# Performance work log

Hardware: AMD Instinct MI355X
Metric: run time of the kernel (lower is better)

The kernel has to match this reference:

```python
import jax, jax.numpy as jnp
import numpy as np
from jax.scipy.special import logsumexp

VOCAB, EMB, SEQ = 100000, 300, 32768
NTAGS = 14          # 12 real tags + START + STOP
START, STOP = 12, 13
NEG = -10000.0


def setup_inputs() -> dict:
    key = jax.random.key(0)
    k0, k1, k2, k3, k4 = jax.random.split(key, 5)
    sentence = jax.random.randint(k0, (SEQ,), 0, VOCAB, dtype=jnp.int32)
    tags = jax.random.randint(k1, (SEQ,), 0, 12, dtype=jnp.int32)  # real tags only
    embeddings = jax.random.normal(k2, (VOCAB, EMB), dtype=jnp.float32)
    W = jax.random.normal(k3, (NTAGS, EMB), dtype=jnp.float32)  # linear2tag, no bias
    transitions = jax.random.normal(k4, (NTAGS, NTAGS), dtype=jnp.float32)
    # match __init__: no transition into START, none out of STOP
    transitions = transitions.at[START, :].set(NEG).at[:, STOP].set(NEG)
    return {"sentence": sentence, "tags": tags, "embeddings": embeddings,
            "W": W, "transitions": transitions}


def _forward_alg(feats, transitions):
    # feats: [L, T]; transitions[next, prev]
    init = jnp.full((NTAGS,), NEG, feats.dtype).at[START].set(0.0)

    def step(fv, feat):
        # alphas[next, prev] = fv[prev] + trans[next, prev] + feat[next]
        alphas = fv[None, :] + transitions + feat[:, None]
        return logsumexp(alphas, axis=1), None

    fv, _ = jax.lax.scan(step, init, feats)
    return logsumexp(fv + transitions[STOP])


def _score_sentence(feats, transitions, tags):
    prev = jnp.concatenate([jnp.array([START], tags.dtype), tags[:-1]])
    trans_score = jnp.sum(transitions[tags, prev])
    emit_score = jnp.sum(jnp.take_along_axis(feats, tags[:, None].astype(jnp.int32), axis=1))
    return trans_score + emit_score + transitions[STOP, tags[-1]]


def _viterbi(feats, transitions):
    init = jnp.full((NTAGS,), NEG, feats.dtype).at[START].set(0.0)

    def step(fv, feat):
        nv = fv[None, :] + transitions          # [next, prev]
        bp = jnp.argmax(nv, axis=1)             # best prev for each next
        return jnp.max(nv, axis=1) + feat, bp

    fv, bps = jax.lax.scan(step, init, feats)   # bps: [L, T]
    terminal = fv + transitions[STOP]
    best_last = jnp.argmax(terminal)
    path_score = terminal[best_last]

    def back(tag, bp):
        return bp[tag], tag                     # emit tag at this position

    _, path = jax.lax.scan(back, best_last, bps, reverse=True)  # [L]
    return path_score, path


def reference(sentence, tags, embeddings, W, transitions):
    # _get_features: embedding lookup + bias-free linear to tag space
    feats = embeddings[sentence] @ W.T                     # [L, T]
    forward_score = _forward_alg(feats, transitions)
    gold_score = _score_sentence(feats, transitions, tags)
    nll = forward_score - gold_score                       # neg_log_likelihood
    path_score, best_path = _viterbi(feats, transitions)   # module.forward
    return nll, path_score, best_path
```

## Files before the change

kernel.cpp:

```cpp
#include <hip/hip_runtime.h>


#define LSEQ    32768
#define NTAGS   14
#define R       12
#define T_START 12
#define T_STOP  13
#define EMBD    300
#define CCH     2048
#define SCH     16
#define NSUP    128
#define NHYP    8

#define OFF_FEATS 0
#define OFF_EXPF  393216
#define OFF_FMAX  786432
#define OFF_PF    819200
#define OFF_PV    1114112
#define OFF_PVC   1409024
#define OFF_BV    1703936
#define OFF_SFX   1728512
#define OFF_GOLD  1753088
#define OFF_SMV   1753104
#define OFF_SMVT  1771536
#define OFF_SMF   1789968
#define OFF_HMV   1808400
#define OFF_HMVT  1809552
#define OFF_HMF   1810704
#define OFF_SBV   1811856
#define OFF_SSFX  1813392
#define OFF_HBV   1814928
#define OFF_HSFX  1815024

__device__ __forceinline__ void load12(const float* __restrict__ p, float* r) {
  const float4* p4 = (const float4*)p;
  float4 a = p4[0], b = p4[1], c = p4[2];
  r[0]=a.x; r[1]=a.y; r[2]=a.z; r[3]=a.w;
  r[4]=b.x; r[5]=b.y; r[6]=b.z; r[7]=b.w;
  r[8]=c.x; r[9]=c.y; r[10]=c.z; r[11]=c.w;
}

__device__ __forceinline__ void lds12(const float* p, float* r) {
  const float4* p4 = (const float4*)p;
  float4 a = p4[0], b = p4[1], c = p4[2];
  r[0]=a.x; r[1]=a.y; r[2]=a.z; r[3]=a.w;
  r[4]=b.x; r[5]=b.y; r[6]=b.z; r[7]=b.w;
  r[8]=c.x; r[9]=c.y; r[10]=c.z; r[11]=c.w;
}

__global__ __launch_bounds__(256) void k_feats(
    const int* __restrict__ sentence, const int* __restrict__ tags,
    const float* __restrict__ emb, const float* __restrict__ W,
    const float* __restrict__ trans, float* __restrict__ ws)
{
  __shared__ float Wl[NTAGS * EMBD];
  __shared__ float gacc;
  for (int i = threadIdx.x; i < NTAGS * EMBD; i += 256) Wl[i] = W[i];
  if (threadIdx.x == 0) gacc = 0.f;
  __syncthreads();

  int grp = threadIdx.x >> 4;
  int g   = threadIdx.x & 15;
  int pos = blockIdx.x * 16 + grp;
  int row = sentence[pos];

  float acc = 0.f;
  if (g < R) {
    const float4* e4 = (const float4*)(emb + (size_t)row * EMBD);
    const float4* w4 = (const float4*)(Wl + g * EMBD);
    #pragma unroll 5
    for (int i = 0; i < EMBD / 4; ++i) {
      float4 a = e4[i]; float4 b = w4[i];
      acc += a.x*b.x + a.y*b.y + a.z*b.z + a.w*b.w;
    }
  }
  float feat = (g < R) ? acc : -3.0e38f;
  float mx = feat;
  #pragma unroll
  for (int off = 1; off < 16; off <<= 1)
    mx = fmaxf(mx, __shfl_xor(mx, off, 16));

  if (g < R) {
    ws[OFF_FEATS + pos * 12 + g] = feat;
    ws[OFF_EXPF  + pos * 12 + g] = __expf(feat - mx);
  }
  if (g == 0) ws[OFF_FMAX + pos] = mx;

  int tg = tags[pos];
  if (g == tg) {
    int prev = (pos == 0) ? T_START : tags[pos - 1];
    float gc = feat + trans[tg * NTAGS + prev];
    if (pos == LSEQ - 1) gc += trans[T_STOP * NTAGS + tg];
    atomicAdd(&gacc, gc);
  }
  __syncthreads();
  if (threadIdx.x == 0) atomicAdd(&ws[OFF_GOLD], gacc);
}

__global__ __launch_bounds__(64) void k_pass1(
    const float* __restrict__ trans, float* __restrict__ ws)
{
  int role = blockIdx.x >> 9;
  int q = threadIdx.x >> 4;
  int p = threadIdx.x & 15;
  int c = (blockIdx.x & 511) * 4 + q;
  int t0 = (c == 0) ? 1 : c * SCH;
  int t1 = c * SCH + SCH;
  bool act = (p < R);

  float Treg[R][R];

  if (role == 0) {
    #pragma unroll
    for (int n = 0; n < R; ++n)
      #pragma unroll
      for (int m = 0; m < R; ++m)
        Treg[n][m] = __expf(trans[n * NTAGS + m]);

    float E[R];
    #pragma unroll
    for (int m = 0; m < R; ++m) E[m] = (m == p) ? 1.f : 0.f;
    int kacc = 0;
    float sfeat = 0.f;

    float ef[R];
    load12(ws + OFF_EXPF + t0 * 12, ef);
    float fm = ws[OFF_FMAX + t0];

    for (int t = t0; t < t1; ++t) {
      float efn[R];
      load12(ws + OFF_EXPF + (t + 1) * 12, efn);
      float fmn = ws[OFF_FMAX + t + 1];
      sfeat += fm;
      float NE[R];
      #pragma unroll
      for (int n = 0; n < R; ++n) {
        float s = Treg[n][0] * E[0];
        #pragma unroll
        for (int m = 1; m < R; ++m) s = fmaf(Treg[n][m], E[m], s);
        NE[n] = s * ef[n];
      }
      #pragma unroll
      for (int n = 0; n < R; ++n) E[n] = NE[n];
      if ((t & 7) == 7) {
        float mx = E[0];
        #pragma unroll
        for (int n = 1; n < R; ++n) mx = fmaxf(mx, E[n]);
        if (mx > 0.f) {
          int k = ((__float_as_int(mx) >> 23) & 0xFF) - 127;
          float sc = __int_as_float((127 - k) << 23);
          #pragma unroll
          for (int n = 0; n < R; ++n) E[n] *= sc;
          kacc += k;
        }
      }
      #pragma unroll
      for (int n = 0; n < R; ++n) ef[n] = efn[n];
      fm = fmn;
    }
    if (act) {
      float base = (float)kacc * 0.6931471805599453f + sfeat;
      #pragma unroll
      for (int n = 0; n < R; ++n) {
        float v = (E[n] > 0.f) ? (__logf(E[n]) + base) : -1.0e30f;
        ws[OFF_PF + c * 144 + n * 12 + p] = v;
      }
    }
  } else {
    #pragma unroll
    for (int n = 0; n < R; ++n)
      #pragma unroll
      for (int m = 0; m < R; ++m)
        Treg[n][m] = trans[n * NTAGS + m];

    float V[R];
    #pragma unroll
    for (int m = 0; m < R; ++m) V[m] = (m == p) ? 0.f : -1.0e30f;

    float fr[R];
    load12(ws + OFF_FEATS + t0 * 12, fr);

    for (int t = t0; t < t1; ++t) {
      float frn[R];
      load12(ws + OFF_FEATS + (t + 1) * 12, frn);
      float NV[R];
      #pragma unroll
      for (int n = 0; n < R; ++n) {
        float b = Treg[n][0] + V[0];
        #pragma unroll
        for (int m = 1; m < R; ++m) b = fmaxf(b, Treg[n][m] + V[m]);
        NV[n] = b + fr[n];
      }
      #pragma unroll
      for (int n = 0; n < R; ++n) { V[n] = NV[n]; fr[n] = frn[n]; }
    }
    if (act) {
      #pragma unroll
      for (int n = 0; n < R; ++n) {
        ws[OFF_PV  + c * 144 + n * 12 + p] = V[n];
        ws[OFF_PVC + c * 144 + p * 12 + n] = V[n];
      }
    }
  }
}

__global__ __launch_bounds__(192) void k_fold(
    float* __restrict__ ws, int srcV, int srcF, int dstV, int dstVT, int dstF)
{
  __shared__ float Ml[144];
  __shared__ float Vl[144];
  int s   = blockIdx.x >> 1;
  int sem = blockIdx.x & 1;
  int l = threadIdx.x;
  bool act = (l < 144);
  int n = l / 12;
  int p = l - n * 12;
  int base = sem ? srcF : srcV;

  float V = (act && n == p) ? 0.f : -1.0e30f;
  float mreg = act ? ws[base + (s * 16) * 144 + l] : 0.f;

  for (int j = 0; j < 16; ++j) {
    if (act) { Ml[l] = mreg; Vl[l] = V; }
    __syncthreads();
    if (act) mreg = ws[base + (s * 16 + j + 1) * 144 + l];
    if (act) {
      if (sem == 0) {
        float best = -3.0e38f;
        #pragma unroll
        for (int m = 0; m < R; ++m)
          best = fmaxf(best, Ml[n * 12 + m] + Vl[m * 12 + p]);
        V = best;
      } else {
        float cand[R]; float mx = -3.0e38f;
        #pragma unroll
        for (int m = 0; m < R; ++m) {
          cand[m] = Ml[n * 12 + m] + Vl[m * 12 + p];
          mx = fmaxf(mx, cand[m]);
        }
        float sum = 0.f;
        #pragma unroll
        for (int m = 0; m < R; ++m) sum += __expf(cand[m] - mx);
        V = mx + __logf(sum);
      }
    }
    __syncthreads();
  }
  if (act) {
    if (sem == 0) {
      ws[dstV  + s * 144 + n * 12 + p] = V;
      ws[dstVT + s * 144 + p * 12 + n] = V;
    } else {
      ws[dstF + s * 144 + n * 12 + p] = V;
    }
  }
}

__global__ __launch_bounds__(192) void k_mid(
    const float* __restrict__ trans, float* __restrict__ ws,
    float* __restrict__ out)
{
  __shared__ float Vsh[3][16];
  int wid  = threadIdx.x >> 6;
  int lane = threadIdx.x & 63;
  int n = lane;
  bool act = (n < R);

  if (wid == 0) {
    float x = -3.0e38f;
    if (act) {
      x = trans[n * NTAGS + T_START] + ws[OFF_FEATS + n];
      ws[OFF_HBV + n] = x;
      Vsh[0][n] = x;
    }
    float row[R], rown[R];
    if (act) load12(ws + OFF_HMV + n * 12, row);
    for (int h = 0; h < NHYP; ++h) {
      if (act) load12(ws + OFF_HMV + (h + 1) * 144 + n * 12, rown);
      float v[R];
      lds12(Vsh[0], v);
      if (act) {
        float nx = row[0] + v[0];
        #pragma unroll
        for (int m = 1; m < R; ++m) nx = fmaxf(nx, row[m] + v[m]);
        if (h < NHYP - 1) ws[OFF_HBV + (h + 1) * 12 + n] = nx;
        Vsh[0][n] = nx;
        #pragma unroll
        for (int m = 0; m < R; ++m) row[m] = rown[m];
      }
    }
    if (lane == 0) {
      float v[R];
      lds12(Vsh[0], v);
      float ps = -3.0e38f;
      #pragma unroll
      for (int m = 0; m < R; ++m) ps = fmaxf(ps, v[m] + trans[T_STOP * NTAGS + m]);
      out[1] = ps;
    }
  } else if (wid == 1) {
    float x = -3.0e38f;
    if (act) {
      x = trans[T_STOP * NTAGS + n];
      ws[OFF_HSFX + (NHYP - 1) * 12 + n] = x;
      Vsh[1][n] = x;
    }
    float row[R], rown[R];
    if (act) load12(ws + OFF_HMVT + (NHYP - 1) * 144 + n * 12, row);
    for (int h = NHYP - 1; h >= 1; --h) {
      if (act) load12(ws + OFF_HMVT + (h - 1) * 144 + n * 12, rown);
      float v[R];
      lds12(Vsh[1], v);
      if (act) {
        float nx = row[0] + v[0];
        #pragma unroll
        for (int m = 1; m < R; ++m) nx = fmaxf(nx, row[m] + v[m]);
        ws[OFF_HSFX + (h - 1) * 12 + n] = nx;
        Vsh[1][n] = nx;
        #pragma unroll
        for (int m = 0; m < R; ++m) row[m] = rown[m];
      }
    }
  } else if (wid == 2) {
    float x = -3.0e38f;
    if (act) {
      x = trans[n * NTAGS + T_START] + ws[OFF_FEATS + n];
      Vsh[2][n] = x;
    }
    float row[R], rown[R];
    if (act) load12(ws + OFF_HMF + n * 12, row);
    for (int h = 0; h < NHYP; ++h) {
      if (act) load12(ws + OFF_HMF + (h + 1) * 144 + n * 12, rown);
      float v[R];
      lds12(Vsh[2], v);
      if (act) {
        float tv[R]; float mx = -3.0e38f;
        #pragma unroll
        for (int m = 0; m < R; ++m) { tv[m] = row[m] + v[m]; mx = fmaxf(mx, tv[m]); }
        float sum = 0.f;
        #pragma unroll
        for (int m = 0; m < R; ++m) sum += __expf(tv[m] - mx);
        Vsh[2][n] = mx + __logf(sum);
        #pragma unroll
        for (int m = 0; m < R; ++m) row[m] = rown[m];
      }
    }
    if (lane == 0) {
      float v[R];
      lds12(Vsh[2], v);
      float mx = -3.0e38f;
      #pragma unroll
      for (int m = 0; m < R; ++m) mx = fmaxf(mx, v[m] + trans[T_STOP * NTAGS + m]);
      float sum = 0.f;
      #pragma unroll
      for (int m = 0; m < R; ++m) sum += __expf(v[m] + trans[T_STOP * NTAGS + m] - mx);
      out[0] = (mx + __logf(sum)) - ws[OFF_GOLD];
    }
  }
}

__global__ __launch_bounds__(64) void k_expandA(
    float* __restrict__ ws)
{
  __shared__ float Vsh[4][16];
  int q = threadIdx.x >> 4;
  int g = threadIdx.x & 15;
  int task = blockIdx.x * 4 + q;
  int h = task >> 1;
  int dir = task & 1;
  bool act = (g < R);

  if (dir == 0) {
    float x = -3.0e38f;
    if (act) {
      x = ws[OFF_HBV + h * 12 + g];
      ws[OFF_SBV + (h * 16) * 12 + g] = x;
      Vsh[q][g] = x;
    }
    float row[R], rown[R];
    if (act) load12(ws + OFF_SMV + (h * 16) * 144 + g * 12, row);
    for (int j = 0; j < 15; ++j) {
      int s = h * 16 + j;
      if (act) load12(ws + OFF_SMV + (s + 1) * 144 + g * 12, rown);
      float v[R];
      lds12(Vsh[q], v);
      if (act) {
        float nx = row[0] + v[0];
        #pragma unroll
        for (int m = 1; m < R; ++m) nx = fmaxf(nx, row[m] + v[m]);
        ws[OFF_SBV + (s + 1) * 12 + g] = nx;
        Vsh[q][g] = nx;
        #pragma unroll
        for (int m = 0; m < R; ++m) row[m] = rown[m];
      }
    }
  } else {
    float x = -3.0e38f;
    if (act) {
      x = ws[OFF_HSFX + h * 12 + g];
      ws[OFF_SSFX + (h * 16 + 15) * 12 + g] = x;
      Vsh[q][g] = x;
    }
    float row[R], rown[R];
    if (act) load12(ws + OFF_SMVT + (h * 16 + 15) * 144 + g * 12, row);
    for (int j = 15; j >= 1; --j) {
      int s = h * 16 + j;
      if (act) load12(ws + OFF_SMVT + (s - 1) * 144 + g * 12, rown);
      float v[R];
      lds12(Vsh[q], v);
      if (act) {
        float nx = row[0] + v[0];
        #pragma unroll
        for (int m = 1; m < R; ++m) nx = fmaxf(nx, row[m] + v[m]);
        ws[OFF_SSFX + (s - 1) * 12 + g] = nx;
        Vsh[q][g] = nx;
        #pragma unroll
        for (int m = 0; m < R; ++m) row[m] = rown[m];
      }
    }
  }
}

__global__ __launch_bounds__(64) void k_expandB(
    float* __restrict__ ws)
{
  __shared__ float Vsh[4][16];
  int q = threadIdx.x >> 4;
  int g = threadIdx.x & 15;
  int task = blockIdx.x * 4 + q;
  int s = task >> 1;
  int dir = task & 1;
  bool act = (g < R);

  if (dir == 0) {
    float x = -3.0e38f;
    if (act) {
      x = ws[OFF_SBV + s * 12 + g];
      ws[OFF_BV + (s * 16) * 12 + g] = x;
      Vsh[q][g] = x;
    }
    float row[R], rown[R];
    if (act) load12(ws + OFF_PV + (s * 16) * 144 + g * 12, row);
    for (int j = 0; j < 15; ++j) {
      int c = s * 16 + j;
      if (act) load12(ws + OFF_PV + (c + 1) * 144 + g * 12, rown);
      float v[R];
      lds12(Vsh[q], v);
      if (act) {
        float nx = row[0] + v[0];
        #pragma unroll
        for (int m = 1; m < R; ++m) nx = fmaxf(nx, row[m] + v[m]);
        ws[OFF_BV + (c + 1) * 12 + g] = nx;
        Vsh[q][g] = nx;
        #pragma unroll
        for (int m = 0; m < R; ++m) row[m] = rown[m];
      }
    }
  } else {
    float x = -3.0e38f;
    if (act) {
      x = ws[OFF_SSFX + s * 12 + g];
      ws[OFF_SFX + (s * 16 + 15) * 12 + g] = x;
      Vsh[q][g] = x;
    }
    float row[R], rown[R];
    if (act) load12(ws + OFF_PVC + (s * 16 + 15) * 144 + g * 12, row);
    for (int j = 15; j >= 1; --j) {
      int c = s * 16 + j;
      if (act) load12(ws + OFF_PVC + (c - 1) * 144 + g * 12, rown);
      float v[R];
      lds12(Vsh[q], v);
      if (act) {
        float nx = row[0] + v[0];
        #pragma unroll
        for (int m = 1; m < R; ++m) nx = fmaxf(nx, row[m] + v[m]);
        ws[OFF_SFX + (c - 1) * 12 + g] = nx;
        Vsh[q][g] = nx;
        #pragma unroll
        for (int m = 0; m < R; ++m) row[m] = rown[m];
      }
    }
  }
}

__global__ __launch_bounds__(64) void k_decode(
    const float* __restrict__ trans, const float* __restrict__ ws,
    float* __restrict__ out)
{
  __shared__ unsigned char bp[4][SCH][16];
  __shared__ float Vsh[4][16];
  int q = threadIdx.x >> 4;
  int g = threadIdx.x & 15;
  int c = blockIdx.x * 4 + q;
  int t0 = (c == 0) ? 1 : c * SCH;
  int t1 = c * SCH + SCH;
  bool act = (g < R);

  float treg[R];
  #pragma unroll
  for (int m = 0; m < R; ++m) treg[m] = act ? trans[g * NTAGS + m] : 0.f;

  float fv = act ? ws[OFF_BV + c * 12 + g] : -3.0e38f;
  Vsh[q][g] = fv;
  float fc = ws[OFF_FEATS + t0 * 12 + g];

  for (int t = t0; t < t1; ++t) {
    float fn = ws[OFF_FEATS + (t + 1) * 12 + g];
    float v[R];
    lds12(Vsh[q], v);
    float best = -3.0e38f; int bi = 0;
    #pragma unroll
    for (int m = 0; m < R; ++m) {
      float cand = treg[m] + v[m];
      if (cand > best) { best = cand; bi = m; }
    }
    float nfv = best + fc;
    if (act) {
      bp[q][t - t0][g] = (unsigned char)bi;
      Vsh[q][g] = nfv;
    }
    fc = fn;
  }

  Vsh[q][g] = act ? (Vsh[q][g] + ws[OFF_SFX + c * 12 + g]) : -3.0e38f;

  if (g == 0) {
    float best = Vsh[q][0]; int idx = 0;
    #pragma unroll
    for (int m = 1; m < R; ++m) {
      float v = Vsh[q][m];
      if (v > best) { best = v; idx = m; }
    }
    int cur = idx;
    int len = t1 - t0;
    out[2 + t0 + len - 1] = (float)cur;
    for (int tt = len - 1; tt >= 1; --tt) {
      cur = bp[q][tt][cur];
      out[2 + t0 + tt - 1] = (float)cur;
    }
    if (c == 0) {
      cur = bp[q][0][cur];
      out[2 + 0] = (float)cur;
    }
  }
}

extern "C" void kernel_launch(void* const* d_in, const int* in_sizes, int n_in,
                              void* d_out, int out_size, void* d_ws, size_t ws_size,
                              hipStream_t stream) {
  (void)in_sizes; (void)n_in; (void)out_size; (void)ws_size;
  const int*   sentence = (const int*)d_in[0];
  const int*   tags     = (const int*)d_in[1];
  const float* emb      = (const float*)d_in[2];
  const float* W        = (const float*)d_in[3];
  const float* trans    = (const float*)d_in[4];
  float* ws  = (float*)d_ws;
  float* out = (float*)d_out;

  hipMemsetAsync(ws + OFF_GOLD, 0, sizeof(float), stream);
  k_feats<<<LSEQ / 16, 256, 0, stream>>>(sentence, tags, emb, W, trans, ws);
  k_pass1<<<1024, 64, 0, stream>>>(trans, ws);
  k_fold<<<NSUP * 2, 192, 0, stream>>>(ws, OFF_PV, OFF_PF, OFF_SMV, OFF_SMVT, OFF_SMF);
  k_fold<<<NHYP * 2, 192, 0, stream>>>(ws, OFF_SMV, OFF_SMF, OFF_HMV, OFF_HMVT, OFF_HMF);
  k_mid<<<1, 192, 0, stream>>>(trans, ws, out);
  k_expandA<<<4, 64, 0, stream>>>(ws);
  k_expandB<<<64, 64, 0, stream>>>(ws);
  k_decode<<<CCH / 4, 64, 0, stream>>>(trans, ws, out);
}
```

Baseline: 274.0 us.

## Fuse post-feature CRF stages into one cooperative kernel with grid syncs

Replaces the seven kernel launches after feature computation (pass1, two folds, mid, two expands, decode) with a single cooperative kernel of 256 blocks that separates the stages with grid.sync(). The gold-score atomic plus its memset are replaced by per-block partial sums that one block reduces inside the mega kernel. The aim is to remove launch gaps and tail latency between many tiny serial kernels. In exchange, grid-wide barriers add their own cost, and the fold stages now run with fewer, larger blocks. The old multi-kernel path is kept as a fallback if the cooperative launch fails.

```diff
diff --git a/kernel.cpp b/kernel.cpp
--- a/kernel.cpp
+++ b/kernel.cpp
@@ -1,4 +1,7 @@
 #include <hip/hip_runtime.h>
+#include <hip/hip_cooperative_groups.h>
+
+namespace cg = cooperative_groups;
 
 
 #define LSEQ    32768
@@ -31,6 +34,7 @@
 #define OFF_SSFX  1813392
 #define OFF_HBV   1814928
 #define OFF_HSFX  1815024
+#define OFF_GOLDP 1815120
 
 __device__ __forceinline__ void load12(const float* __restrict__ p, float* r) {
   const float4* p4 = (const float4*)p;
@@ -94,7 +98,495 @@
     atomicAdd(&gacc, gc);
   }
   __syncthreads();
-  if (threadIdx.x == 0) atomicAdd(&ws[OFF_GOLD], gacc);
+  if (threadIdx.x == 0) ws[OFF_GOLDP + blockIdx.x] = gacc;
+}
+
+__device__ __forceinline__ void fold16(
+    float* __restrict__ ws, float* Ml, float* Vl, int tid, int s, int sem,
+    int srcV, int srcF, int dstV, int dstVT, int dstF)
+{
+  int l = tid;
+  bool act = (l < 144);
+  int n = l / 12;
+  int p = l - n * 12;
+  int base = sem ? srcF : srcV;
+
+  float V = (act && n == p) ? 0.f : -1.0e30f;
+  float mreg = act ? ws[base + (s * 16) * 144 + l] : 0.f;
+
+  for (int j = 0; j < 16; ++j) {
+    if (act) { Ml[l] = mreg; Vl[l] = V; }
+    __syncthreads();
+    if (act) mreg = ws[base + (s * 16 + j + 1) * 144 + l];
+    if (act) {
+      if (sem == 0) {
+        float best = -3.0e38f;
+        #pragma unroll
+        for (int m = 0; m < R; ++m)
+          best = fmaxf(best, Ml[n * 12 + m] + Vl[m * 12 + p]);
+        V = best;
+      } else {
+        float cand[R]; float mx = -3.0e38f;
+        #pragma unroll
+        for (int m = 0; m < R; ++m) {
+          cand[m] = Ml[n * 12 + m] + Vl[m * 12 + p];
+          mx = fmaxf(mx, cand[m]);
+        }
+        float sum = 0.f;
+        #pragma unroll
+        for (int m = 0; m < R; ++m) sum += __expf(cand[m] - mx);
+        V = mx + __logf(sum);
+      }
+    }
+    __syncthreads();
+  }
+  if (act) {
+    if (sem == 0) {
+      ws[dstV  + s * 144 + n * 12 + p] = V;
+      ws[dstVT + s * 144 + p * 12 + n] = V;
+    } else {
+      ws[dstF + s * 144 + n * 12 + p] = V;
+    }
+  }
+}
+
+__global__ __launch_bounds__(256) void k_mega(
+    const float* __restrict__ trans, float* __restrict__ ws,
+    float* __restrict__ out)
+{
+  cg::grid_group grid = cg::this_grid();
+  const int tid = threadIdx.x;
+  const int bid = blockIdx.x;
+
+  __shared__ float Ml[144];
+  __shared__ float Vl[144];
+  __shared__ float Vmid[3][16];
+  __shared__ float VexA[4][16];
+  __shared__ float VexB[4][16];
+  __shared__ float Vdec[8][16];
+  __shared__ unsigned char bpd[8][SCH][16];
+  __shared__ float gsh[256];
+
+  {
+    int gw   = bid * 4 + (tid >> 6);
+    int lane = tid & 63;
+    int role = gw >> 9;
+    int q = lane >> 4;
+    int p = lane & 15;
+    int c = (gw & 511) * 4 + q;
+    int t0 = (c == 0) ? 1 : c * SCH;
+    int t1 = c * SCH + SCH;
+    bool act = (p < R);
+
+    float Treg[R][R];
+
+    if (role == 0) {
+      #pragma unroll
+      for (int n = 0; n < R; ++n)
+        #pragma unroll
+        for (int m = 0; m < R; ++m)
+          Treg[n][m] = __expf(trans[n * NTAGS + m]);
+
+      float E[R];
+      #pragma unroll
+      for (int m = 0; m < R; ++m) E[m] = (m == p) ? 1.f : 0.f;
+      int kacc = 0;
+      float sfeat = 0.f;
+
+      float ef[R];
+      load12(ws + OFF_EXPF + t0 * 12, ef);
+      float fm = ws[OFF_FMAX + t0];
+
+      for (int t = t0; t < t1; ++t) {
+        float efn[R];
+        load12(ws + OFF_EXPF + (t + 1) * 12, efn);
+        float fmn = ws[OFF_FMAX + t + 1];
+        sfeat += fm;
+        float NE[R];
+        #pragma unroll
+        for (int n = 0; n < R; ++n) {
+          float s = Treg[n][0] * E[0];
+          #pragma unroll
+          for (int m = 1; m < R; ++m) s = fmaf(Treg[n][m], E[m], s);
+          NE[n] = s * ef[n];
+        }
+        #pragma unroll
+        for (int n = 0; n < R; ++n) E[n] = NE[n];
+        if ((t & 7) == 7) {
+          float mx = E[0];
+          #pragma unroll
+          for (int n = 1; n < R; ++n) mx = fmaxf(mx, E[n]);
+          if (mx > 0.f) {
+            int k = ((__float_as_int(mx) >> 23) & 0xFF) - 127;
+            float sc = __int_as_float((127 - k) << 23);
+            #pragma unroll
+            for (int n = 0; n < R; ++n) E[n] *= sc;
+            kacc += k;
+          }
+        }
+        #pragma unroll
+        for (int n = 0; n < R; ++n) ef[n] = efn[n];
+        fm = fmn;
+      }
+      if (act) {
+        float base = (float)kacc * 0.6931471805599453f + sfeat;
+        #pragma unroll
+        for (int n = 0; n < R; ++n) {
+          float v = (E[n] > 0.f) ? (__logf(E[n]) + base) : -1.0e30f;
+          ws[OFF_PF + c * 144 + n * 12 + p] = v;
+        }
+      }
+    } else {
+      #pragma unroll
+      for (int n = 0; n < R; ++n)
+        #pragma unroll
+        for (int m = 0; m < R; ++m)
+          Treg[n][m] = trans[n * NTAGS + m];
+
+      float V[R];
+      #pragma unroll
+      for (int m = 0; m < R; ++m) V[m] = (m == p) ? 0.f : -1.0e30f;
+
+      float fr[R];
+      load12(ws + OFF_FEATS + t0 * 12, fr);
+
+      for (int t = t0; t < t1; ++t) {
+        float frn[R];
+        load12(ws + OFF_FEATS + (t + 1) * 12, frn);
+        float NV[R];
+        #pragma unroll
+        for (int n = 0; n < R; ++n) {
+          float b = Treg[n][0] + V[0];
+          #pragma unroll
+          for (int m = 1; m < R; ++m) b = fmaxf(b, Treg[n][m] + V[m]);
+          NV[n] = b + fr[n];
+        }
+        #pragma unroll
+        for (int n = 0; n < R; ++n) { V[n] = NV[n]; fr[n] = frn[n]; }
+      }
+      if (act) {
+        #pragma unroll
+        for (int n = 0; n < R; ++n) {
+          ws[OFF_PV  + c * 144 + n * 12 + p] = V[n];
+          ws[OFF_PVC + c * 144 + p * 12 + n] = V[n];
+        }
+      }
+    }
+  }
+  grid.sync();
+
+  fold16(ws, Ml, Vl, tid, bid >> 1, bid & 1,
+         OFF_PV, OFF_PF, OFF_SMV, OFF_SMVT, OFF_SMF);
+  grid.sync();
+
+  if (bid < 16) {
+    fold16(ws, Ml, Vl, tid, bid >> 1, bid & 1,
+           OFF_SMV, OFF_SMF, OFF_HMV, OFF_HMVT, OFF_HMF);
+  } else if (bid == 16) {
+    float s = 0.f;
+    for (int i = tid; i < CCH; i += 256) s += ws[OFF_GOLDP + i];
+    gsh[tid] = s;
+    __syncthreads();
+    for (int off = 128; off > 0; off >>= 1) {
+      if (tid < off) gsh[tid] += gsh[tid + off];
+      __syncthreads();
+    }
+    if (tid == 0) ws[OFF_GOLD] = gsh[0];
+  }
+  grid.sync();
+
+  if (bid == 0) {
+    int wid  = tid >> 6;
+    int lane = tid & 63;
+    int n = lane;
+    bool act = (n < R);
+
+    if (wid == 0) {
+      float x = -3.0e38f;
+      if (act) {
+        x = trans[n * NTAGS + T_START] + ws[OFF_FEATS + n];
+        ws[OFF_HBV + n] = x;
+        Vmid[0][n] = x;
+      }
+      float row[R], rown[R];
+      if (act) load12(ws + OFF_HMV + n * 12, row);
+      for (int h = 0; h < NHYP; ++h) {
+        if (act) load12(ws + OFF_HMV + (h + 1) * 144 + n * 12, rown);
+        float v[R];
+        lds12(Vmid[0], v);
+        if (act) {
+          float nx = row[0] + v[0];
+          #pragma unroll
+          for (int m = 1; m < R; ++m) nx = fmaxf(nx, row[m] + v[m]);
+          if (h < NHYP - 1) ws[OFF_HBV + (h + 1) * 12 + n] = nx;
+          Vmid[0][n] = nx;
+          #pragma unroll
+          for (int m = 0; m < R; ++m) row[m] = rown[m];
+        }
+      }
+      if (lane == 0) {
+        float v[R];
+        lds12(Vmid[0], v);
+        float ps = -3.0e38f;
+        #pragma unroll
+        for (int m = 0; m < R; ++m) ps = fmaxf(ps, v[m] + trans[T_STOP * NTAGS + m]);
+        out[1] = ps;
+      }
+    } else if (wid == 1) {
+      float x = -3.0e38f;
+      if (act) {
+        x = trans[T_STOP * NTAGS + n];
+        ws[OFF_HSFX + (NHYP - 1) * 12 + n] = x;
+        Vmid[1][n] = x;
+      }
+      float row[R], rown[R];
+      if (act) load12(ws + OFF_HMVT + (NHYP - 1) * 144 + n * 12, row);
+      for (int h = NHYP - 1; h >= 1; --h) {
+        if (act) load12(ws + OFF_HMVT + (h - 1) * 144 + n * 12, rown);
+        float v[R];
+        lds12(Vmid[1], v);
+        if (act) {
+          float nx = row[0] + v[0];
+          #pragma unroll
+          for (int m = 1; m < R; ++m) nx = fmaxf(nx, row[m] + v[m]);
+          ws[OFF_HSFX + (h - 1) * 12 + n] = nx;
+          Vmid[1][n] = nx;
+          #pragma unroll
+          for (int m = 0; m < R; ++m) row[m] = rown[m];
+        }
+      }
+    } else if (wid == 2) {
+      float x = -3.0e38f;
+      if (act) {
+        x = trans[n * NTAGS + T_START] + ws[OFF_FEATS + n];
+        Vmid[2][n] = x;
+      }
+      float row[R], rown[R];
+      if (act) load12(ws + OFF_HMF + n * 12, row);
+      for (int h = 0; h < NHYP; ++h) {
+        if (act) load12(ws + OFF_HMF + (h + 1) * 144 + n * 12, rown);
+        float v[R];
+        lds12(Vmid[2], v);
+        if (act) {
+          float tv[R]; float mx = -3.0e38f;
+          #pragma unroll
+          for (int m = 0; m < R; ++m) { tv[m] = row[m] + v[m]; mx = fmaxf(mx, tv[m]); }
+          float sum = 0.f;
+          #pragma unroll
+          for (int m = 0; m < R; ++m) sum += __expf(tv[m] - mx);
+          Vmid[2][n] = mx + __logf(sum);
+          #pragma unroll
+          for (int m = 0; m < R; ++m) row[m] = rown[m];
+        }
+      }
+      if (lane == 0) {
+        float v[R];
+        lds12(Vmid[2], v);
+        float mx = -3.0e38f;
+        #pragma unroll
+        for (int m = 0; m < R; ++m) mx = fmaxf(mx, v[m] + trans[T_STOP * NTAGS + m]);
+        float sum = 0.f;
+        #pragma unroll
+        for (int m = 0; m < R; ++m) sum += __expf(v[m] + trans[T_STOP * NTAGS + m] - mx);
+        out[0] = (mx + __logf(sum)) - ws[OFF_GOLD];
+      }
+    }
+  }
+  grid.sync();
+
+  if (bid < 4 && tid < 64) {
+    int q = tid >> 4;
+    int g = tid & 15;
+    int task = bid * 4 + q;
+    int h = task >> 1;
+    int dir = task & 1;
+    bool act = (g < R);
+
+    if (dir == 0) {
+      float x = -3.0e38f;
+      if (act) {
+        x = ws[OFF_HBV + h * 12 + g];
+        ws[OFF_SBV + (h * 16) * 12 + g] = x;
+        VexA[q][g] = x;
+      }
+      float row[R], rown[R];
+      if (act) load12(ws + OFF_SMV + (h * 16) * 144 + g * 12, row);
+      for (int j = 0; j < 15; ++j) {
+        int s = h * 16 + j;
+        if (act) load12(ws + OFF_SMV + (s + 1) * 144 + g * 12, rown);
+        float v[R];
+        lds12(VexA[q], v);
+        if (act) {
+          float nx = row[0] + v[0];
+          #pragma unroll
+          for (int m = 1; m < R; ++m) nx = fmaxf(nx, row[m] + v[m]);
+          ws[OFF_SBV + (s + 1) * 12 + g] = nx;
+          VexA[q][g] = nx;
+          #pragma unroll
+          for (int m = 0; m < R; ++m) row[m] = rown[m];
+        }
+      }
+    } else {
+      float x = -3.0e38f;
+      if (act) {
+        x = ws[OFF_HSFX + h * 12 + g];
+        ws[OFF_SSFX + (h * 16 + 15) * 12 + g] = x;
+        VexA[q][g] = x;
+      }
+      float row[R], rown[R];
+      if (act) load12(ws + OFF_SMVT + (h * 16 + 15) * 144 + g * 12, row);
+      for (int j = 15; j >= 1; --j) {
+        int s = h * 16 + j;
+        if (act) load12(ws + OFF_SMVT + (s - 1) * 144 + g * 12, rown);
+        float v[R];
+        lds12(VexA[q], v);
+        if (act) {
+          float nx = row[0] + v[0];
+          #pragma unroll
+          for (int m = 1; m < R; ++m) nx = fmaxf(nx, row[m] + v[m]);
+          ws[OFF_SSFX + (s - 1) * 12 + g] = nx;
+          VexA[q][g] = nx;
+          #pragma unroll
+          for (int m = 0; m < R; ++m) row[m] = rown[m];
+        }
+      }
+    }
+  }
+  grid.sync();
+
+  if (bid < 64 && tid < 64) {
+    int q = tid >> 4;
+    int g = tid & 15;
+    int task = bid * 4 + q;
+    int s = task >> 1;
+    int dir = task & 1;
+    bool act = (g < R);
+
+    if (dir == 0) {
+      float x = -3.0e38f;
+      if (act) {
+        x = ws[OFF_SBV + s * 12 + g];
+        ws[OFF_BV + (s * 16) * 12 + g] = x;
+        VexB[q][g] = x;
+      }
+      float row[R], rown[R];
+      if (act) load12(ws + OFF_PV + (s * 16) * 144 + g * 12, row);
+      for (int j = 0; j < 15; ++j) {
+        int c = s * 16 + j;
+        if (act) load12(ws + OFF_PV + (c + 1) * 144 + g * 12, rown);
+        float v[R];
+        lds12(VexB[q], v);
+        if (act) {
+          float nx = row[0] + v[0];
+          #pragma unroll
+          for (int m = 1; m < R; ++m) nx = fmaxf(nx, row[m] + v[m]);
+          ws[OFF_BV + (c + 1) * 12 + g] = nx;
+          VexB[q][g] = nx;
+          #pragma unroll
+          for (int m = 0; m < R; ++m) row[m] = rown[m];
+        }
+      }
+    } else {
+      float x = -3.0e38f;
+      if (act) {
+        x = ws[OFF_SSFX + s * 12 + g];
+        ws[OFF_SFX + (s * 16 + 15) * 12 + g] = x;
+        VexB[q][g] = x;
+      }
+      float row[R], rown[R];
+      if (act) load12(ws + OFF_PVC + (s * 16 + 15) * 144 + g * 12, row);
+      for (int j = 15; j >= 1; --j) {
+        int c = s * 16 + j;
+        if (act) load12(ws + OFF_PVC + (c - 1) * 144 + g * 12, rown);
+        float v[R];
+        lds12(VexB[q], v);
+        if (act) {
+          float nx = row[0] + v[0];
+          #pragma unroll
+          for (int m = 1; m < R; ++m) nx = fmaxf(nx, row[m] + v[m]);
+          ws[OFF_SFX + (c - 1) * 12 + g] = nx;
+          VexB[q][g] = nx;
+          #pragma unroll
+          for (int m = 0; m < R; ++m) row[m] = rown[m];
+        }
+      }
+    }
+  }
+  grid.sync();
+
+  {
+    int q = tid >> 4;
+    int g = tid & 15;
+    if (q < 8) {
+      int c = bid * 8 + q;
+      int t0 = (c == 0) ? 1 : c * SCH;
+      int t1 = c * SCH + SCH;
+      bool act = (g < R);
+
+      float treg[R];
+      #pragma unroll
+      for (int m = 0; m < R; ++m) treg[m] = act ? trans[g * NTAGS + m] : 0.f;
+
+      float fv = act ? ws[OFF_BV + c * 12 + g] : -3.0e38f;
+      Vdec[q][g] = fv;
+      float fc = ws[OFF_FEATS + t0 * 12 + g];
+
+      for (int t = t0; t < t1; ++t) {
+        float fn = ws[OFF_FEATS + (t + 1) * 12 + g];
+        float v[R];
+        lds12(Vdec[q], v);
+        float best = -3.0e38f; int bi = 0;
+        #pragma unroll
+        for (int m = 0; m < R; ++m) {
+          float cand = treg[m] + v[m];
+          if (cand > best) { best = cand; bi = m; }
+        }
+        float nfv = best + fc;
+        if (act) {
+          bpd[q][t - t0][g] = (unsigned char)bi;
+          Vdec[q][g] = nfv;
+        }
+        fc = fn;
+      }
+
+      Vdec[q][g] = act ? (Vdec[q][g] + ws[OFF_SFX + c * 12 + g]) : -3.0e38f;
+
+      if (g == 0) {
+        float best = Vdec[q][0]; int idx = 0;
+        #pragma unroll
+        for (int m = 1; m < R; ++m) {
+          float v = Vdec[q][m];
+          if (v > best) { best = v; idx = m; }
+        }
+        int cur = idx;
+        int len = t1 - t0;
+        out[2 + t0 + len - 1] = (float)cur;
+        for (int tt = len - 1; tt >= 1; --tt) {
+          cur = bpd[q][tt][cur];
+          out[2 + t0 + tt - 1] = (float)cur;
+        }
+        if (c == 0) {
+          cur = bpd[q][0][cur];
+          out[2 + 0] = (float)cur;
+        }
+      }
+    }
+  }
+}
+
+
+__global__ __launch_bounds__(256) void k_goldsum(float* __restrict__ ws)
+{
+  __shared__ float gsh[256];
+  float s = 0.f;
+  for (int i = threadIdx.x; i < CCH; i += 256) s += ws[OFF_GOLDP + i];
+  gsh[threadIdx.x] = s;
+  __syncthreads();
+  for (int off = 128; off > 0; off >>= 1) {
+    if (threadIdx.x < off) gsh[threadIdx.x] += gsh[threadIdx.x + off];
+    __syncthreads();
+  }
+  if (threadIdx.x == 0) ws[OFF_GOLD] = gsh[0];
 }
 
 __global__ __launch_bounds__(64) void k_pass1(
@@ -556,13 +1048,19 @@
   float* ws  = (float*)d_ws;
   float* out = (float*)d_out;
 
-  hipMemsetAsync(ws + OFF_GOLD, 0, sizeof(float), stream);
   k_feats<<<LSEQ / 16, 256, 0, stream>>>(sentence, tags, emb, W, trans, ws);
-  k_pass1<<<1024, 64, 0, stream>>>(trans, ws);
-  k_fold<<<NSUP * 2, 192, 0, stream>>>(ws, OFF_PV, OFF_PF, OFF_SMV, OFF_SMVT, OFF_SMF);
-  k_fold<<<NHYP * 2, 192, 0, stream>>>(ws, OFF_SMV, OFF_SMF, OFF_HMV, OFF_HMVT, OFF_HMF);
-  k_mid<<<1, 192, 0, stream>>>(trans, ws, out);
-  k_expandA<<<4, 64, 0, stream>>>(ws);
-  k_expandB<<<64, 64, 0, stream>>>(ws);
-  k_decode<<<CCH / 4, 64, 0, stream>>>(trans, ws, out);
-}
+
+  void* kargs[] = { (void*)&trans, (void*)&ws, (void*)&out };
+  hipError_t ce = hipLaunchCooperativeKernel((const void*)k_mega, dim3(256),
+                                             dim3(256), kargs, 0, stream);
+  if (ce != hipSuccess) {
+    k_goldsum<<<1, 256, 0, stream>>>(ws);
+    k_pass1<<<1024, 64, 0, stream>>>(trans, ws);
+    k_fold<<<NSUP * 2, 192, 0, stream>>>(ws, OFF_PV, OFF_PF, OFF_SMV, OFF_SMVT, OFF_SMF);
+    k_fold<<<NHYP * 2, 192, 0, stream>>>(ws, OFF_SMV, OFF_SMF, OFF_HMV, OFF_HMVT, OFF_HMF);
+    k_mid<<<1, 192, 0, stream>>>(trans, ws, out);
+    k_expandA<<<4, 64, 0, stream>>>(ws);
+    k_expandB<<<64, 64, 0, stream>>>(ws);
+    k_decode<<<CCH / 4, 64, 0, stream>>>(trans, ws, out);
+  }
+}
```

Result: slower. 430.1 us (+57.0%).

## Fuse mid/expand/decode kernels, stage fold matrices in LDS, drop gold atomics

Applied to the files above, without the earlier changes.

Merges the single-block mid kernel with the first expand stage, and the second expand stage with the Viterbi decode, keeping intermediate boundary vectors in shared memory instead of global workspace. The fold kernel now loads all 16 matrices per block into LDS up front instead of one per step. The global atomic gold-score accumulation and its memset are replaced with per-block partials that are reduced inside the mid kernel. The aim is fewer kernel launches and less global round-trip latency on the serial chain. In exchange, the decode stage runs with fewer, larger blocks, and the expand work inside each block is serialized before the decode.

```diff
diff --git a/kernel.cpp b/kernel.cpp
--- a/kernel.cpp
+++ b/kernel.cpp
@@ -31,6 +31,7 @@
 #define OFF_SSFX  1813392
 #define OFF_HBV   1814928
 #define OFF_HSFX  1815024
+#define OFF_GOLDP 1815120
 
 __device__ __forceinline__ void load12(const float* __restrict__ p, float* r) {
   const float4* p4 = (const float4*)p;
@@ -94,7 +95,7 @@
     atomicAdd(&gacc, gc);
   }
   __syncthreads();
-  if (threadIdx.x == 0) atomicAdd(&ws[OFF_GOLD], gacc);
+  if (threadIdx.x == 0) ws[OFF_GOLDP + blockIdx.x] = gacc;
 }
 
 __global__ __launch_bounds__(64) void k_pass1(
@@ -204,10 +205,10 @@
   }
 }
 
-__global__ __launch_bounds__(192) void k_fold(
+__global__ __launch_bounds__(192) void k_foldS(
     float* __restrict__ ws, int srcV, int srcF, int dstV, int dstVT, int dstF)
 {
-  __shared__ float Ml[144];
+  __shared__ float Msh[16 * 144];
   __shared__ float Vl[144];
   int s   = blockIdx.x >> 1;
   int sem = blockIdx.x & 1;
@@ -217,25 +218,30 @@
   int p = l - n * 12;
   int base = sem ? srcF : srcV;
 
+  const float4* src4 = (const float4*)(ws + base + s * (16 * 144));
+  float4* d4 = (float4*)Msh;
+  #pragma unroll
+  for (int i = 0; i < 3; ++i) d4[l + i * 192] = src4[l + i * 192];
+
   float V = (act && n == p) ? 0.f : -1.0e30f;
-  float mreg = act ? ws[base + (s * 16) * 144 + l] : 0.f;
+  __syncthreads();
 
   for (int j = 0; j < 16; ++j) {
-    if (act) { Ml[l] = mreg; Vl[l] = V; }
+    if (act) Vl[l] = V;
     __syncthreads();
-    if (act) mreg = ws[base + (s * 16 + j + 1) * 144 + l];
     if (act) {
+      const float* M = Msh + j * 144 + n * 12;
       if (sem == 0) {
         float best = -3.0e38f;
         #pragma unroll
         for (int m = 0; m < R; ++m)
-          best = fmaxf(best, Ml[n * 12 + m] + Vl[m * 12 + p]);
+          best = fmaxf(best, M[m] + Vl[m * 12 + p]);
         V = best;
       } else {
         float cand[R]; float mx = -3.0e38f;
         #pragma unroll
         for (int m = 0; m < R; ++m) {
-          cand[m] = Ml[n * 12 + m] + Vl[m * 12 + p];
+          cand[m] = M[m] + Vl[m * 12 + p];
           mx = fmaxf(mx, cand[m]);
         }
         float sum = 0.f;
@@ -256,82 +262,89 @@
   }
 }
 
-__global__ __launch_bounds__(192) void k_mid(
+__global__ __launch_bounds__(256) void k_midexpA(
     const float* __restrict__ trans, float* __restrict__ ws,
     float* __restrict__ out)
 {
-  __shared__ float Vsh[3][16];
-  int wid  = threadIdx.x >> 6;
-  int lane = threadIdx.x & 63;
-  int n = lane;
-  bool act = (n < R);
+  __shared__ float hbv_sh[NHYP][12];
+  __shared__ float hsfx_sh[NHYP][12];
+  __shared__ float Vm[3][16];
+  __shared__ float VexA[16][16];
+  __shared__ float gold_sh, lse_sh;
+
+  int tid  = threadIdx.x;
+  int wid  = tid >> 6;
+  int lane = tid & 63;
 
   if (wid == 0) {
+    int n = lane; bool act = (n < R);
     float x = -3.0e38f;
     if (act) {
       x = trans[n * NTAGS + T_START] + ws[OFF_FEATS + n];
-      ws[OFF_HBV + n] = x;
-      Vsh[0][n] = x;
+      hbv_sh[0][n] = x;
+      Vm[0][n] = x;
     }
     float row[R], rown[R];
     if (act) load12(ws + OFF_HMV + n * 12, row);
     for (int h = 0; h < NHYP; ++h) {
       if (act) load12(ws + OFF_HMV + (h + 1) * 144 + n * 12, rown);
       float v[R];
-      lds12(Vsh[0], v);
+      lds12(Vm[0], v);
       if (act) {
         float nx = row[0] + v[0];
         #pragma unroll
         for (int m = 1; m < R; ++m) nx = fmaxf(nx, row[m] + v[m]);
-        if (h < NHYP - 1) ws[OFF_HBV + (h + 1) * 12 + n] = nx;
-        Vsh[0][n] = nx;
+        if (h < NHYP - 1) hbv_sh[h + 1][n] = nx;
+        Vm[0][n] = nx;
         #pragma unroll
         for (int m = 0; m < R; ++m) row[m] = rown[m];
       }
     }
     if (lane == 0) {
       float v[R];
-      lds12(Vsh[0], v);
+      lds12(Vm[0], v);
       float ps = -3.0e38f;
       #pragma unroll
       for (int m = 0; m < R; ++m) ps = fmaxf(ps, v[m] + trans[T_STOP * NTAGS + m]);
       out[1] = ps;
     }
   } else if (wid == 1) {
+    int n = lane; bool act = (n < R);
     float x = -3.0e38f;
     if (act) {
       x = trans[T_STOP * NTAGS + n];
-      ws[OFF_HSFX + (NHYP - 1) * 12 + n] = x;
-      Vsh[1][n] = x;
+      hsfx_sh[NHYP - 1][n] = x;
+      Vm[1][n] = x;
     }
     float row[R], rown[R];
     if (act) load12(ws + OFF_HMVT + (NHYP - 1) * 144 + n * 12, row);
     for (int h = NHYP - 1; h >= 1; --h) {
       if (act) load12(ws + OFF_HMVT + (h - 1) * 144 + n * 12, rown);
       float v[R];
-      lds12(Vsh[1], v);
+      lds12(Vm[1], v);
       if (act) {
         float nx = row[0] + v[0];
         #pragma unroll
         for (int m = 1; m < R; ++m) nx = fmaxf(nx, row[m] + v[m]);
-        ws[OFF_HSFX + (h - 1) * 12 + n] = nx;
-        Vsh[1][n] = nx;
+        hsfx_sh[h - 1][n] = nx;
+        Vm[1][n] = nx;
         #pragma unroll
         for (int m = 0; m < R; ++m) row[m] = rown[m];
       }
     }
   } else if (wid == 2) {
+    int n = lane; bool act = (n < R);
     float x = -3.0e38f;
     if (act) {
       x = trans[n * NTAGS + T_START] + ws[OFF_FEATS + n];
-      Vsh[2][n] = x;
+      Vm[2][n] = x;
     }
     float row[R], rown[R];
     if (act) load12(ws + OFF_HMF + n * 12, row);
     for (int h = 0; h < NHYP; ++h) {
       if (act) load12(ws + OFF_HMF + (h + 1) * 144 + n * 12, rown);
       float v[R];
-      lds12(Vsh[2], v);
+      lds12(Vm[2], v);
       if (act) {
         float tv[R]; float mx = -3.0e38f;
         #pragma unroll
@@ -339,207 +352,199 @@
         float sum = 0.f;
         #pragma unroll
         for (int m = 0; m < R; ++m) sum += __expf(tv[m] - mx);
-        Vsh[2][n] = mx + __logf(sum);
+        Vm[2][n] = mx + __logf(sum);
         #pragma unroll
         for (int m = 0; m < R; ++m) row[m] = rown[m];
       }
     }
     if (lane == 0) {
       float v[R];
-      lds12(Vsh[2], v);
+      lds12(Vm[2], v);
       float mx = -3.0e38f;
       #pragma unroll
       for (int m = 0; m < R; ++m) mx = fmaxf(mx, v[m] + trans[T_STOP * NTAGS + m]);
       float sum = 0.f;
       #pragma unroll
       for (int m = 0; m < R; ++m) sum += __expf(v[m] + trans[T_STOP * NTAGS + m] - mx);
-      out[0] = (mx + __logf(sum)) - ws[OFF_GOLD];
-    }
-  }
-}
-
-__global__ __launch_bounds__(64) void k_expandA(
-    float* __restrict__ ws)
+      lse_sh = mx + __logf(sum);
+    }
+  } else {
+    float s = 0.f;
+    for (int i = lane; i < CCH; i += 64) s += ws[OFF_GOLDP + i];
+    #pragma unroll
+    for (int off = 32; off > 0; off >>= 1) s += __shfl_xor(s, off);
+    if (lane == 0) gold_sh = s;
+  }
+  __syncthreads();
+
+  if (tid == 0) out[0] = lse_sh - gold_sh;
+
+  {
+    int dir  = tid >> 7;
+    int h    = (tid >> 4) & 7;
+    int g    = tid & 15;
+    int task = tid >> 4;
+    bool act = (g < R);
+
+    if (dir == 0) {
+      float x = -3.0e38f;
+      if (act) {
+        x = hbv_sh[h][g];
+        ws[OFF_SBV + (h * 16) * 12 + g] = x;
+        VexA[task][g] = x;
+      }
+      float row[R], rown[R];
+      if (act) load12(ws + OFF_SMV + (h * 16) * 144 + g * 12, row);
+      for (int j = 0; j < 15; ++j) {
+        int s = h * 16 + j;
+        if (act) load12(ws + OFF_SMV + (s + 1) * 144 + g * 12, rown);
+        float v[R];
+        lds12(VexA[task], v);
+        if (act) {
+          float nx = row[0] + v[0];
+          #pragma unroll
+          for (int m = 1; m < R; ++m) nx = fmaxf(nx, row[m] + v[m]);
+          ws[OFF_SBV + (s + 1) * 12 + g] = nx;
+          VexA[task][g] = nx;
+          #pragma unroll
+          for (int m = 0; m < R; ++m) row[m] = rown[m];
+        }
+      }
+    } else {
+      float x = -3.0e38f;
+      if (act) {
+        x = hsfx_sh[h][g];
+        ws[OFF_SSFX + (h * 16 + 15) * 12 + g] = x;
+        VexA[task][g] = x;
+      }
+      float row[R], rown[R];
+      if (act) load12(ws + OFF_SMVT + (h * 16 + 15) * 144 + g * 12, row);
+      for (int j = 15; j >= 1; --j) {
+        int s = h * 16 + j;
+        if (act) load12(ws + OFF_SMVT + (s - 1) * 144 + g * 12, rown);
+        float v[R];
+        lds12(VexA[task], v);
+        if (act) {
+          float nx = row[0] + v[0];
+          #pragma unroll
+          for (int m = 1; m < R; ++m) nx = fmaxf(nx, row[m] + v[m]);
+          ws[OFF_SSFX + (s - 1) * 12 + g] = nx;
+          VexA[task][g] = nx;
+          #pragma unroll
+          for (int m = 0; m < R; ++m) row[m] = rown[m];
+        }
+      }
+    }
+  }
+}
+
+__global__ __launch_bounds__(256) void k_expBdec(
+    const float* __restrict__ trans, const float* __restrict__ ws,
+    float* __restrict__ out)
 {
-  __shared__ float Vsh[4][16];
-  int q = threadIdx.x >> 4;
-  int g = threadIdx.x & 15;
-  int task = blockIdx.x * 4 + q;
-  int h = task >> 1;
-  int dir = task & 1;
-  bool act = (g < R);
-
-  if (dir == 0) {
+  __shared__ float bv_sh[SCH][12];
+  __shared__ float sfx_sh[SCH][12];
+  __shared__ float Vdec[SCH][16];
+  __shared__ unsigned char bpd[SCH][SCH][16];
+
+  int tid = threadIdx.x;
+  int s   = blockIdx.x;
+
+  if (tid < 16) {
+    int g = tid; bool act = (g < R);
     float x = -3.0e38f;
-    if (act) {
-      x = ws[OFF_HBV + h * 12 + g];
-      ws[OFF_SBV + (h * 16) * 12 + g] = x;
-      Vsh[q][g] = x;
-    }
-    float row[R], rown[R];
-    if (act) load12(ws + OFF_SMV + (h * 16) * 144 + g * 12, row);
-    for (int j = 0; j < 15; ++j) {
-      int s = h * 16 + j;
-      if (act) load12(ws + OFF_SMV + (s + 1) * 144 + g * 12, rown);
-      float v[R];
-      lds12(Vsh[q], v);
-      if (act) {
-        float nx = row[0] + v[0];
-        #pragma unroll
-        for (int m = 1; m < R; ++m) nx = fmaxf(nx, row[m] + v[m]);
-        ws[OFF_SBV + (s + 1) * 12 + g] = nx;
-        Vsh[q][g] = nx;
-        #pragma unroll
-        for (int m = 0; m < R; ++m) row[m] = rown[m];
-      }
-    }
-  } else {
-    float x = -3.0e38f;
-    if (act) {
-      x = ws[OFF_HSFX + h * 12 + g];
-      ws[OFF_SSFX + (h * 16 + 15) * 12 + g] = x;
-      Vsh[q][g] = x;
-    }
-    float row[R], rown[R];
-    if (act) load12(ws + OFF_SMVT + (h * 16 + 15) * 144 + g * 12, row);
-    for (int j = 15; j >= 1; --j) {
-      int s = h * 16 + j;
-      if (act) load12(ws + OFF_SMVT + (s - 1) * 144 + g * 12, rown);
-      float v[R];
-      lds12(Vsh[q], v);
-      if (act) {
-        float nx = row[0] + v[0];
-        #pragma unroll
-        for (int m = 1; m < R; ++m) nx = fmaxf(nx, row[m] + v[m]);
-        ws[OFF_SSFX + (s - 1) * 12 + g] = nx;
-        Vsh[q][g] = nx;
-        #pragma unroll
-        for (int m = 0; m < R; ++m) row[m] = rown[m];
-      }
-    }
-  }
-}
-
-__global__ __launch_bounds__(64) void k_expandB(
-    float* __restrict__ ws)
-{
-  __shared__ float Vsh[4][16];
-  int q = threadIdx.x >> 4;
-  int g = threadIdx.x & 15;
-  int task = blockIdx.x * 4 + q;
-  int s = task >> 1;
-  int dir = task & 1;
-  bool act = (g < R);
-
-  if (dir == 0) {
-    float x = -3.0e38f;
-    if (act) {
-      x = ws[OFF_SBV + s * 12 + g];
-      ws[OFF_BV + (s * 16) * 12 + g] = x;
-      Vsh[q][g] = x;
-    }
+    if (act) { x = ws[OFF_SBV + s * 12 + g]; bv_sh[0][g] = x; }
     float row[R], rown[R];
     if (act) load12(ws + OFF_PV + (s * 16) * 144 + g * 12, row);
     for (int j = 0; j < 15; ++j) {
-      int c = s * 16 + j;
-      if (act) load12(ws + OFF_PV + (c + 1) * 144 + g * 12, rown);
-      float v[R];
-      lds12(Vsh[q], v);
+      if (act) load12(ws + OFF_PV + (s * 16 + j + 1) * 144 + g * 12, rown);
+      float v[R];
+      lds12(bv_sh[j], v);
       if (act) {
         float nx = row[0] + v[0];
         #pragma unroll
         for (int m = 1; m < R; ++m) nx = fmaxf(nx, row[m] + v[m]);
-        ws[OFF_BV + (c + 1) * 12 + g] = nx;
-        Vsh[q][g] = nx;
+        bv_sh[j + 1][g] = nx;
         #pragma unroll
         for (int m = 0; m < R; ++m) row[m] = rown[m];
       }
     }
-  } else {
+  } else if (tid >= 64 && tid < 80) {
+    int g = tid - 64; bool act = (g < R);
     float x = -3.0e38f;
-    if (act) {
-      x = ws[OFF_SSFX + s * 12 + g];
-      ws[OFF_SFX + (s * 16 + 15) * 12 + g] = x;
-      Vsh[q][g] = x;
-    }
+    if (act) { x = ws[OFF_SSFX + s * 12 + g]; sfx_sh[SCH - 1][g] = x; }
     float row[R], rown[R];
     if (act) load12(ws + OFF_PVC + (s * 16 + 15) * 144 + g * 12, row);
     for (int j = 15; j >= 1; --j) {
-      int c = s * 16 + j;
-      if (act) load12(ws + OFF_PVC + (c - 1) * 144 + g * 12, rown);
-      float v[R];
-      lds12(Vsh[q], v);
+      if (act) load12(ws + OFF_PVC + (s * 16 + j - 1) * 144 + g * 12, rown);
+      float v[R];
+      lds12(sfx_sh[j], v);
       if (act) {
         float nx = row[0] + v[0];
         #pragma unroll
         for (int m = 1; m < R; ++m) nx = fmaxf(nx, row[m] + v[m]);
-        ws[OFF_SFX + (c - 1) * 12 + g] = nx;
-        Vsh[q][g] = nx;
+        sfx_sh[j - 1][g] = nx;
         #pragma unroll
         for (int m = 0; m < R; ++m) row[m] = rown[m];
       }
     }
   }
-}
-
-__global__ __launch_bounds__(64) void k_decode(
-    const float* __restrict__ trans, const float* __restrict__ ws,
-    float* __restrict__ out)
-{
-  __shared__ unsigned char bp[4][SCH][16];
-  __shared__ float Vsh[4][16];
-  int q = threadIdx.x >> 4;
-  int g = threadIdx.x & 15;
-  int c = blockIdx.x * 4 + q;
-  int t0 = (c == 0) ? 1 : c * SCH;
-  int t1 = c * SCH + SCH;
-  bool act = (g < R);
-
-  float treg[R];
-  #pragma unroll
-  for (int m = 0; m < R; ++m) treg[m] = act ? trans[g * NTAGS + m] : 0.f;
-
-  float fv = act ? ws[OFF_BV + c * 12 + g] : -3.0e38f;
-  Vsh[q][g] = fv;
-  float fc = ws[OFF_FEATS + t0 * 12 + g];
-
-  for (int t = t0; t < t1; ++t) {
-    float fn = ws[OFF_FEATS + (t + 1) * 12 + g];
-    float v[R];
-    lds12(Vsh[q], v);
-    float best = -3.0e38f; int bi = 0;
+  __syncthreads();
+
+  {
+    int q = tid >> 4;
+    int g = tid & 15;
+    int c = s * 16 + q;
+    int t0 = (c == 0) ? 1 : c * SCH;
+    int t1 = c * SCH + SCH;
+    bool act = (g < R);
+
+    float treg[R];
     #pragma unroll
-    for (int m = 0; m < R; ++m) {
-      float cand = treg[m] + v[m];
-      if (cand > best) { best = cand; bi = m; }
-    }
-    float nfv = best + fc;
-    if (act) {
-      bp[q][t - t0][g] = (unsigned char)bi;
-      Vsh[q][g] = nfv;
-    }
-    fc = fn;
-  }
-
-  Vsh[q][g] = act ? (Vsh[q][g] + ws[OFF_SFX + c * 12 + g]) : -3.0e38f;
-
-  if (g == 0) {
-    float best = Vsh[q][0]; int idx = 0;
-    #pragma unroll
-    for (int m = 1; m < R; ++m) {
-      float v = Vsh[q][m];
-      if (v > best) { best = v; idx = m; }
-    }
-    int cur = idx;
-    int len = t1 - t0;
-    out[2 + t0 + len - 1] = (float)cur;
-    for (int tt = len - 1; tt >= 1; --tt) {
-      cur = bp[q][tt][cur];
-      out[2 + t0 + tt - 1] = (float)cur;
-    }
-    if (c == 0) {
-      cur = bp[q][0][cur];
-      out[2 + 0] = (float)cur;
+    for (int m = 0; m < R; ++m) treg[m] = act ? trans[g * NTAGS + m] : 0.f;
+
+    float fv = act ? bv_sh[q][g] : -3.0e38f;
+    Vdec[q][g] = fv;
+    float fc = ws[OFF_FEATS + t0 * 12 + g];
+
+    for (int t = t0; t < t1; ++t) {
+      float fn = ws[OFF_FEATS + (t + 1) * 12 + g];
+      float v[R];
+      lds12(Vdec[q], v);
+      float best = -3.0e38f; int bi = 0;
+      #pragma unroll
+      for (int m = 0; m < R; ++m) {
+        float cand = treg[m] + v[m];
+        if (cand > best) { best = cand; bi = m; }
+      }
+      float nfv = best + fc;
+      if (act) {
+        bpd[q][t - t0][g] = (unsigned char)bi;
+        Vdec[q][g] = nfv;
+      }
+      fc = fn;
+    }
+
+    Vdec[q][g] = act ? (Vdec[q][g] + sfx_sh[q][g]) : -3.0e38f;
+
+    if (g == 0) {
+      float best = Vdec[q][0]; int idx = 0;
+      #pragma unroll
+      for (int m = 1; m < R; ++m) {
+        float v = Vdec[q][m];
+        if (v > best) { best = v; idx = m; }
+      }
+      int cur = idx;
+      int len = t1 - t0;
+      out[2 + t0 + len - 1] = (float)cur;
+      for (int tt = len - 1; tt >= 1; --tt) {
+        cur = bpd[q][tt][cur];
+        out[2 + t0 + tt - 1] = (float)cur;
+      }
+      if (c == 0) {
+        cur = bpd[q][0][cur];
+        out[2 + 0] = (float)cur;
+      }
     }
   }
 }
@@ -556,13 +561,10 @@
   float* ws  = (float*)d_ws;
   float* out = (float*)d_out;
 
-  hipMemsetAsync(ws + OFF_GOLD, 0, sizeof(float), stream);
   k_feats<<<LSEQ / 16, 256, 0, stream>>>(sentence, tags, emb, W, trans, ws);
   k_pass1<<<1024, 64, 0, stream>>>(trans, ws);
-  k_fold<<<NSUP * 2, 192, 0, stream>>>(ws, OFF_PV, OFF_PF, OFF_SMV, OFF_SMVT, OFF_SMF);
-  k_fold<<<NHYP * 2, 192, 0, stream>>>(ws, OFF_SMV, OFF_SMF, OFF_HMV, OFF_HMVT, OFF_HMF);
-  k_mid<<<1, 192, 0, stream>>>(trans, ws, out);
-  k_expandA<<<4, 64, 0, stream>>>(ws);
-  k_expandB<<<64, 64, 0, stream>>>(ws);
-  k_decode<<<CCH / 4, 64, 0, stream>>>(trans, ws, out);
-}
+  k_foldS<<<NSUP * 2, 192, 0, stream>>>(ws, OFF_PV, OFF_PF, OFF_SMV, OFF_SMVT, OFF_SMF);
+  k_foldS<<<NHYP * 2, 192, 0, stream>>>(ws, OFF_SMV, OFF_SMF, OFF_HMV, OFF_HMVT, OFF_HMF);
+  k_midexpA<<<1, 256, 0, stream>>>(trans, ws, out);
+  k_expBdec<<<NSUP, 256, 0, stream>>>(trans, ws, out);
+}
```

After: 244.4 us. -10.8%, faster.
